# Optimization experiments

Hardware: AMD Instinct MI355X
Metric: run time of the kernel (lower is better)

Reference implementation:

```python
import jax, jax.numpy as jnp
import numpy as np

NOISE_EPS = 0.01
TOP_K = 2


def setup_inputs() -> dict:
    key = jax.random.key(0)
    k1, k2, k3, k4 = jax.random.split(key, 4)
    B, S, D, E = 4, 4096, 2048, 64
    x = jax.random.normal(k1, (B, S, D), dtype=jnp.float32)
    raw_noise = jax.random.normal(k2, (B, S, E), dtype=jnp.float32)
    # gating_mlp: single Linear(D -> E), init std=0.02, zero bias
    W_gate = 0.02 * jax.random.normal(k3, (E, D), dtype=jnp.float32)
    b_gate = jnp.zeros((E,), dtype=jnp.float32)
    # noise_projection: Linear(D -> E, bias=False), init std=1/sqrt(D)
    W_noise = (1.0 / np.sqrt(D)) * jax.random.normal(k4, (E, D), dtype=jnp.float32)
    return {"x": x, "raw_noise": raw_noise, "W_gate": W_gate, "b_gate": b_gate, "W_noise": W_noise}


def reference(x, raw_noise, W_gate, b_gate, W_noise):
    # gate logits: [B,S,E]
    logits = jnp.einsum("bsd,ed->bse", x, W_gate) + b_gate
    # noisy top-k routing (training path)
    noise_stddev = jax.nn.softplus(jnp.einsum("bsd,ed->bse", x, W_noise)) + NOISE_EPS
    noisy = logits + raw_noise * noise_stddev
    top_v, top_i = jax.lax.top_k(noisy, TOP_K)            # [B,S,K]
    top_p = jax.nn.softmax(top_v.astype(jnp.float32), axis=-1).astype(noisy.dtype)
    B, S, E = noisy.shape
    T = B * S
    flat_logits = noisy.reshape(T, E)
    flat_i = top_i.reshape(T, TOP_K)
    flat_p = top_p.reshape(T, TOP_K)
    sparse = jnp.zeros((T, E), dtype=noisy.dtype).at[jnp.arange(T)[:, None], flat_i].set(flat_p)
    # aux load-balancing loss
    indicator = (sparse > 0.0).astype(jnp.float32)
    fraction_routed = indicator.sum(axis=0) / T           # f_e
    router_probs = jax.nn.softmax(flat_logits.astype(jnp.float32), axis=-1)
    avg_prob = router_probs.mean(axis=0)                  # p_e
    aux_loss = jnp.sum(fraction_routed * avg_prob) * E
    return sparse.reshape(B, S, E), aux_loss.astype(noisy.dtype)
```

## Files before the change

### kernel.cpp

```cpp
#include <hip/hip_runtime.h>
#include <math.h>

#define TOK 16384
#define DD  2048
#define EE  64
#define MT  64
#define BKC 32
#define NKC 64
#define LDA 40

typedef _Float16 half8 __attribute__((ext_vector_type(8)));
typedef float floatx4 __attribute__((ext_vector_type(4)));

__global__ void build_wf(const float* __restrict__ Wg, const float* __restrict__ Wn,
                         _Float16* __restrict__ wf) {
  int tid  = blockIdx.x * 256 + threadIdx.x;
  int lane = tid & 63;
  int kc   = (tid >> 6) & 63;
  int ct   = tid >> 12;
  int col  = (ct & 3) * 16 + (lane & 15);
  int k    = kc * 32 + (lane >> 4) * 8;
  const float* W = (ct < 4) ? Wg : Wn;
  const float* src = W + (size_t)col * DD + k;
  float4 a = *reinterpret_cast<const float4*>(src);
  float4 b = *reinterpret_cast<const float4*>(src + 4);
  float v[8] = {a.x, a.y, a.z, a.w, b.x, b.y, b.z, b.w};
  half8 hi, lo;
#pragma unroll
  for (int j = 0; j < 8; ++j) {
    _Float16 h = (_Float16)v[j];
    hi[j] = h;
    lo[j] = (_Float16)(v[j] - (float)h);
  }
  size_t base = (((size_t)(ct * 64 + kc) * 2 + 0) * 64 + lane) * 8;
  *reinterpret_cast<half8*>(wf + base)       = hi;
  *reinterpret_cast<half8*>(wf + base + 512) = lo;
}

__global__ __launch_bounds__(256, 1)
void gating_kernel(const float* __restrict__ x, const float* __restrict__ rn,
                   const _Float16* __restrict__ wf, const float* __restrict__ bg,
                   float* __restrict__ out,
                   float* __restrict__ cnt_g, float* __restrict__ psum_g) {
  __shared__ _Float16 xs[2][2][MT * LDA];
  __shared__ float Lb[MT][129];
  __shared__ float Pb[MT][65];
  __shared__ float Rb[MT][65];
  __shared__ float Sb[MT * EE];
  __shared__ float Bgs[EE];
  __shared__ float isum[MT];
  __shared__ int   ti[MT][2];

  const int t  = threadIdx.x;
  const int w  = t >> 6;
  const int l  = t & 63;
  const int q  = l >> 4;
  const int cl = l & 15;
  const int t0 = blockIdx.x * MT;

  const int stok = t >> 2;
  const int skof = (t & 3) * 8;
  const float* xrow = x + (size_t)(t0 + stok) * DD + skof;

  floatx4 acc[4][2];
#pragma unroll
  for (int mt = 0; mt < 4; ++mt)
#pragma unroll
    for (int nt = 0; nt < 2; ++nt) acc[mt][nt] = (floatx4)0.f;

  const half8* wfp = (const half8*)wf;
  half8 Bc[2][2], Bn[2][2];

  {
    float4 a = *reinterpret_cast<const float4*>(xrow);
    float4 b = *reinterpret_cast<const float4*>(xrow + 4);
    float v[8] = {a.x, a.y, a.z, a.w, b.x, b.y, b.z, b.w};
    half8 hi, lo;
#pragma unroll
    for (int j = 0; j < 8; ++j) {
      _Float16 h = (_Float16)v[j];
      hi[j] = h;
      lo[j] = (_Float16)(v[j] - (float)h);
    }
    *reinterpret_cast<half8*>(&xs[0][0][stok * LDA + skof]) = hi;
    *reinterpret_cast<half8*>(&xs[0][1][stok * LDA + skof]) = lo;
#pragma unroll
    for (int nt = 0; nt < 2; ++nt) {
      int ct = w * 2 + nt;
#pragma unroll
      for (int s = 0; s < 2; ++s)
        Bc[nt][s] = wfp[((size_t)(ct * 64 + 0) * 2 + s) * 64 + l];
    }
  }

  for (int kc = 0; kc < NKC; ++kc) {
    const int cur = kc & 1;
    float4 pa, pb;
    const bool more = (kc < NKC - 1);
    if (more) {
      pa = *reinterpret_cast<const float4*>(xrow + (kc + 1) * BKC);
      pb = *reinterpret_cast<const float4*>(xrow + (kc + 1) * BKC + 4);
#pragma unroll
      for (int nt = 0; nt < 2; ++nt) {
        int ct = w * 2 + nt;
#pragma unroll
        for (int s = 0; s < 2; ++s)
          Bn[nt][s] = wfp[((size_t)(ct * 64 + kc + 1) * 2 + s) * 64 + l];
      }
    }
    __syncthreads();

    half8 Ah[4], Al[4];
#pragma unroll
    for (int mt = 0; mt < 4; ++mt) {
      Ah[mt] = *reinterpret_cast<const half8*>(&xs[cur][0][(mt * 16 + cl) * LDA + q * 8]);
      Al[mt] = *reinterpret_cast<const half8*>(&xs[cur][1][(mt * 16 + cl) * LDA + q * 8]);
    }
#pragma unroll
    for (int mt = 0; mt < 4; ++mt)
#pragma unroll
      for (int nt = 0; nt < 2; ++nt)
        acc[mt][nt] = __builtin_amdgcn_mfma_f32_16x16x32_f16(Ah[mt], Bc[nt][0], acc[mt][nt], 0, 0, 0);
#pragma unroll
    for (int mt = 0; mt < 4; ++mt)
#pragma unroll
      for (int nt = 0; nt < 2; ++nt)
        acc[mt][nt] = __builtin_amdgcn_mfma_f32_16x16x32_f16(Ah[mt], Bc[nt][1], acc[mt][nt], 0, 0, 0);
#pragma unroll
    for (int mt = 0; mt < 4; ++mt)
#pragma unroll
      for (int nt = 0; nt < 2; ++nt)
        acc[mt][nt] = __builtin_amdgcn_mfma_f32_16x16x32_f16(Al[mt], Bc[nt][0], acc[mt][nt], 0, 0, 0);

    if (more) {
      float v[8] = {pa.x, pa.y, pa.z, pa.w, pb.x, pb.y, pb.z, pb.w};
      half8 hi, lo;
#pragma unroll
      for (int j = 0; j < 8; ++j) {
        _Float16 h = (_Float16)v[j];
        hi[j] = h;
        lo[j] = (_Float16)(v[j] - (float)h);
      }
      *reinterpret_cast<half8*>(&xs[cur ^ 1][0][stok * LDA + skof]) = hi;
      *reinterpret_cast<half8*>(&xs[cur ^ 1][1][stok * LDA + skof]) = lo;
#pragma unroll
      for (int nt = 0; nt < 2; ++nt)
#pragma unroll
        for (int s = 0; s < 2; ++s) Bc[nt][s] = Bn[nt][s];
    }
  }

#pragma unroll
  for (int mt = 0; mt < 4; ++mt)
#pragma unroll
    for (int nt = 0; nt < 2; ++nt)
#pragma unroll
      for (int r = 0; r < 4; ++r)
        Lb[mt * 16 + q * 4 + r][w * 32 + nt * 16 + cl] = acc[mt][nt][r];

  if (t < EE) Bgs[t] = bg[t];
#pragma unroll
  for (int i = 0; i < 16; ++i) Sb[t + 256 * i] = 0.f;
#pragma unroll
  for (int i = 0; i < 16; ++i) {
    int idx = t + 256 * i;
    Rb[idx >> 6][idx & 63] = rn[(size_t)t0 * EE + idx];
  }
  __syncthreads();

  if (t < MT) {
    float v1 = -1e30f, v2 = -1e30f;
    int   i1 = 0, i2 = 0;
    float s = 0.f;
    for (int e = 0; e < EE; ++e) {
      float g  = Lb[t][e] + Bgs[e];
      float h  = Lb[t][EE + e];
      float sp = (h > 20.f) ? h : log1pf(expf(h));
      float v  = g + Rb[t][e] * (sp + 0.01f);
      float ev = expf(v);
      s += ev;
      Pb[t][e] = ev;
      if (v > v1)      { v2 = v1; i2 = i1; v1 = v; i1 = e; }
      else if (v > v2) { v2 = v;  i2 = e; }
    }
    isum[t] = 1.f / s;
    ti[t][0] = i1; ti[t][1] = i2;
    float e2 = expf(v2 - v1);
    float dn = 1.f + e2;
    Sb[t * EE + i1] = 1.f / dn;
    Sb[t * EE + i2] = e2 / dn;
  }
  __syncthreads();

#pragma unroll
  for (int i = 0; i < 16; ++i)
    out[(size_t)t0 * EE + t + 256 * i] = Sb[t + 256 * i];

  if (t < EE) {
    float s = 0.f;
    int   c = 0;
#pragma unroll
    for (int m = 0; m < MT; ++m) {
      s += Pb[m][t] * isum[m];
      c += (ti[m][0] == t) + (ti[m][1] == t);
    }
    atomicAdd(&psum_g[t], s);
    atomicAdd(&cnt_g[t], (float)c);
  }
}

__global__ void aux_kernel(const float* __restrict__ cnt_g,
                           const float* __restrict__ psum_g,
                           float* __restrict__ out) {
  int e = threadIdx.x;
  float v = cnt_g[e] * psum_g[e];
#pragma unroll
  for (int o = 32; o > 0; o >>= 1) v += __shfl_down(v, o);
  if (e == 0)
    out[(size_t)TOK * EE] = v * ((float)EE / ((float)TOK * (float)TOK));
}

extern "C" void kernel_launch(void* const* d_in, const int* in_sizes, int n_in,
                              void* d_out, int out_size, void* d_ws, size_t ws_size,
                              hipStream_t stream) {
  const float* x  = (const float*)d_in[0];
  const float* rn = (const float*)d_in[1];
  const float* Wg = (const float*)d_in[2];
  const float* bg = (const float*)d_in[3];
  const float* Wn = (const float*)d_in[4];
  float* out    = (float*)d_out;
  float* cnt_g  = (float*)d_ws;
  float* psum_g = cnt_g + EE;
  _Float16* wf  = (_Float16*)((float*)d_ws + 128);

  hipMemsetAsync(d_ws, 0, 2 * EE * sizeof(float), stream);
  build_wf<<<128, 256, 0, stream>>>(Wg, Wn, wf);
  gating_kernel<<<TOK / MT, 256, 0, stream>>>(x, rn, wf, bg, out, cnt_g, psum_g);
  aux_kernel<<<1, 64, 0, stream>>>(cnt_g, psum_g, out);
}
```

Before: 249.4 us.

## Halve token tile, fuse gating epilogue into registers, and raise occupancy

Shrinks the token tile from 64 to 32, which doubles the block count to 512, cuts shared memory through an aliased smem buffer, and sets launch bounds to two blocks per CU so more waves can hide latency. The per-element softplus, noise and exp work now runs in the MFMA accumulator registers across all threads instead of a serial 64-thread loop. The dense output is written with vectorized stores computed from top-k indices. Each block still reads the full weight panel, so weight traffic per token doubles, and the 16-wide column mapping changes the channel layout.

```diff
diff --git a/kernel.cpp b/kernel.cpp
--- a/kernel.cpp
+++ b/kernel.cpp
@@ -4,13 +4,14 @@
 #define TOK 16384
 #define DD  2048
 #define EE  64
-#define MT  64
+#define MT  32
 #define BKC 32
 #define NKC 64
 #define LDA 40
 
-typedef _Float16 half8 __attribute__((ext_vector_type(8)));
-typedef float floatx4 __attribute__((ext_vector_type(4)));
+typedef _Float16 half4v __attribute__((ext_vector_type(4)));
+typedef _Float16 half8  __attribute__((ext_vector_type(8)));
+typedef float    floatx4 __attribute__((ext_vector_type(4)));
 
 __global__ void build_wf(const float* __restrict__ Wg, const float* __restrict__ Wn,
                          _Float16* __restrict__ wf) {
@@ -37,34 +38,42 @@
   *reinterpret_cast<half8*>(wf + base + 512) = lo;
 }
 
-__global__ __launch_bounds__(256, 1)
+__global__ __launch_bounds__(256, 2)
 void gating_kernel(const float* __restrict__ x, const float* __restrict__ rn,
                    const _Float16* __restrict__ wf, const float* __restrict__ bg,
                    float* __restrict__ out,
                    float* __restrict__ cnt_g, float* __restrict__ psum_g) {
-  __shared__ _Float16 xs[2][2][MT * LDA];
-  __shared__ float Lb[MT][129];
-  __shared__ float Pb[MT][65];
-  __shared__ float Rb[MT][65];
-  __shared__ float Sb[MT * EE];
-  __shared__ float Bgs[EE];
-  __shared__ float isum[MT];
-  __shared__ int   ti[MT][2];
+  __shared__ char smem[17536];
+  _Float16* xs  = (_Float16*)smem;
+  float*    Vb  = (float*)smem;
+  float*    Eb  = (float*)(smem + 8448);
+  float*    isum= (float*)(smem + 16896);
+  int*      ti  = (int*)(smem + 17024);
+  float*    tp  = (float*)(smem + 17280);
 
   const int t  = threadIdx.x;
   const int w  = t >> 6;
   const int l  = t & 63;
   const int q  = l >> 4;
   const int cl = l & 15;
+  const int c  = w * 16 + cl;
   const int t0 = blockIdx.x * MT;
 
-  const int stok = t >> 2;
-  const int skof = (t & 3) * 8;
+  const int stok = t >> 3;
+  const int skof = (t & 7) * 4;
   const float* xrow = x + (size_t)(t0 + stok) * DD + skof;
 
-  floatx4 acc[4][2];
-#pragma unroll
-  for (int mt = 0; mt < 4; ++mt)
+  const float bgv = bg[c];
+  float rnv[2][4];
+#pragma unroll
+  for (int mt = 0; mt < 2; ++mt)
+#pragma unroll
+    for (int r = 0; r < 4; ++r)
+      rnv[mt][r] = rn[(size_t)(t0 + mt * 16 + q * 4 + r) * EE + c];
+
+  floatx4 acc[2][2];
+#pragma unroll
+  for (int mt = 0; mt < 2; ++mt)
 #pragma unroll
     for (int nt = 0; nt < 2; ++nt) acc[mt][nt] = (floatx4)0.f;
 
@@ -73,20 +82,19 @@
 
   {
     float4 a = *reinterpret_cast<const float4*>(xrow);
-    float4 b = *reinterpret_cast<const float4*>(xrow + 4);
-    float v[8] = {a.x, a.y, a.z, a.w, b.x, b.y, b.z, b.w};
-    half8 hi, lo;
-#pragma unroll
-    for (int j = 0; j < 8; ++j) {
+    float v[4] = {a.x, a.y, a.z, a.w};
+    half4v hi, lo;
+#pragma unroll
+    for (int j = 0; j < 4; ++j) {
       _Float16 h = (_Float16)v[j];
       hi[j] = h;
       lo[j] = (_Float16)(v[j] - (float)h);
     }
-    *reinterpret_cast<half8*>(&xs[0][0][stok * LDA + skof]) = hi;
-    *reinterpret_cast<half8*>(&xs[0][1][stok * LDA + skof]) = lo;
+    *reinterpret_cast<half4v*>(&xs[(0 * 2 + 0) * MT * LDA + stok * LDA + skof]) = hi;
+    *reinterpret_cast<half4v*>(&xs[(0 * 2 + 1) * MT * LDA + stok * LDA + skof]) = lo;
 #pragma unroll
     for (int nt = 0; nt < 2; ++nt) {
-      int ct = w * 2 + nt;
+      const int ct = w + nt * 4;
 #pragma unroll
       for (int s = 0; s < 2; ++s)
         Bc[nt][s] = wfp[((size_t)(ct * 64 + 0) * 2 + s) * 64 + l];
@@ -95,14 +103,13 @@
 
   for (int kc = 0; kc < NKC; ++kc) {
     const int cur = kc & 1;
-    float4 pa, pb;
     const bool more = (kc < NKC - 1);
+    float4 pa;
     if (more) {
       pa = *reinterpret_cast<const float4*>(xrow + (kc + 1) * BKC);
-      pb = *reinterpret_cast<const float4*>(xrow + (kc + 1) * BKC + 4);
 #pragma unroll
       for (int nt = 0; nt < 2; ++nt) {
-        int ct = w * 2 + nt;
+        const int ct = w + nt * 4;
 #pragma unroll
         for (int s = 0; s < 2; ++s)
           Bn[nt][s] = wfp[((size_t)(ct * 64 + kc + 1) * 2 + s) * 64 + l];
@@ -110,39 +117,41 @@
     }
     __syncthreads();
 
-    half8 Ah[4], Al[4];
-#pragma unroll
-    for (int mt = 0; mt < 4; ++mt) {
-      Ah[mt] = *reinterpret_cast<const half8*>(&xs[cur][0][(mt * 16 + cl) * LDA + q * 8]);
-      Al[mt] = *reinterpret_cast<const half8*>(&xs[cur][1][(mt * 16 + cl) * LDA + q * 8]);
-    }
-#pragma unroll
-    for (int mt = 0; mt < 4; ++mt)
+    half8 Ah[2], Al[2];
+#pragma unroll
+    for (int mt = 0; mt < 2; ++mt) {
+      Ah[mt] = *reinterpret_cast<const half8*>(
+          &xs[(cur * 2 + 0) * MT * LDA + (mt * 16 + cl) * LDA + q * 8]);
+      Al[mt] = *reinterpret_cast<const half8*>(
+          &xs[(cur * 2 + 1) * MT * LDA + (mt * 16 + cl) * LDA + q * 8]);
+    }
+#pragma unroll
+    for (int mt = 0; mt < 2; ++mt)
 #pragma unroll
       for (int nt = 0; nt < 2; ++nt)
         acc[mt][nt] = __builtin_amdgcn_mfma_f32_16x16x32_f16(Ah[mt], Bc[nt][0], acc[mt][nt], 0, 0, 0);
 #pragma unroll
-    for (int mt = 0; mt < 4; ++mt)
+    for (int mt = 0; mt < 2; ++mt)
 #pragma unroll
       for (int nt = 0; nt < 2; ++nt)
         acc[mt][nt] = __builtin_amdgcn_mfma_f32_16x16x32_f16(Ah[mt], Bc[nt][1], acc[mt][nt], 0, 0, 0);
 #pragma unroll
-    for (int mt = 0; mt < 4; ++mt)
+    for (int mt = 0; mt < 2; ++mt)
 #pragma unroll
       for (int nt = 0; nt < 2; ++nt)
         acc[mt][nt] = __builtin_amdgcn_mfma_f32_16x16x32_f16(Al[mt], Bc[nt][0], acc[mt][nt], 0, 0, 0);
 
     if (more) {
-      float v[8] = {pa.x, pa.y, pa.z, pa.w, pb.x, pb.y, pb.z, pb.w};
-      half8 hi, lo;
-#pragma unroll
-      for (int j = 0; j < 8; ++j) {
+      float v[4] = {pa.x, pa.y, pa.z, pa.w};
+      half4v hi, lo;
+#pragma unroll
+      for (int j = 0; j < 4; ++j) {
         _Float16 h = (_Float16)v[j];
         hi[j] = h;
         lo[j] = (_Float16)(v[j] - (float)h);
       }
-      *reinterpret_cast<half8*>(&xs[cur ^ 1][0][stok * LDA + skof]) = hi;
-      *reinterpret_cast<half8*>(&xs[cur ^ 1][1][stok * LDA + skof]) = lo;
+      *reinterpret_cast<half4v*>(&xs[((cur ^ 1) * 2 + 0) * MT * LDA + stok * LDA + skof]) = hi;
+      *reinterpret_cast<half4v*>(&xs[((cur ^ 1) * 2 + 1) * MT * LDA + stok * LDA + skof]) = lo;
 #pragma unroll
       for (int nt = 0; nt < 2; ++nt)
 #pragma unroll
@@ -150,22 +159,20 @@
     }
   }
 
-#pragma unroll
-  for (int mt = 0; mt < 4; ++mt)
-#pragma unroll
-    for (int nt = 0; nt < 2; ++nt)
-#pragma unroll
-      for (int r = 0; r < 4; ++r)
-        Lb[mt * 16 + q * 4 + r][w * 32 + nt * 16 + cl] = acc[mt][nt][r];
-
-  if (t < EE) Bgs[t] = bg[t];
-#pragma unroll
-  for (int i = 0; i < 16; ++i) Sb[t + 256 * i] = 0.f;
-#pragma unroll
-  for (int i = 0; i < 16; ++i) {
-    int idx = t + 256 * i;
-    Rb[idx >> 6][idx & 63] = rn[(size_t)t0 * EE + idx];
-  }
+  __syncthreads();
+
+#pragma unroll
+  for (int mt = 0; mt < 2; ++mt)
+#pragma unroll
+    for (int r = 0; r < 4; ++r) {
+      const int tk = mt * 16 + q * 4 + r;
+      float g  = acc[mt][0][r] + bgv;
+      float h  = acc[mt][1][r];
+      float sp = (h > 20.f) ? h : log1pf(expf(h));
+      float v  = g + rnv[mt][r] * (sp + 0.01f);
+      Vb[tk * 66 + c] = v;
+      Eb[tk * 66 + c] = expf(v);
+    }
   __syncthreads();
 
   if (t < MT) {
@@ -173,39 +180,46 @@
     int   i1 = 0, i2 = 0;
     float s = 0.f;
     for (int e = 0; e < EE; ++e) {
-      float g  = Lb[t][e] + Bgs[e];
-      float h  = Lb[t][EE + e];
-      float sp = (h > 20.f) ? h : log1pf(expf(h));
-      float v  = g + Rb[t][e] * (sp + 0.01f);
-      float ev = expf(v);
-      s += ev;
-      Pb[t][e] = ev;
+      float v = Vb[t * 66 + e];
+      s += Eb[t * 66 + e];
       if (v > v1)      { v2 = v1; i2 = i1; v1 = v; i1 = e; }
       else if (v > v2) { v2 = v;  i2 = e; }
     }
     isum[t] = 1.f / s;
-    ti[t][0] = i1; ti[t][1] = i2;
+    ti[t * 2 + 0] = i1; ti[t * 2 + 1] = i2;
     float e2 = expf(v2 - v1);
     float dn = 1.f + e2;
-    Sb[t * EE + i1] = 1.f / dn;
-    Sb[t * EE + i2] = e2 / dn;
+    tp[t * 2 + 0] = 1.f / dn;
+    tp[t * 2 + 1] = e2 / dn;
   }
   __syncthreads();
 
-#pragma unroll
-  for (int i = 0; i < 16; ++i)
-    out[(size_t)t0 * EE + t + 256 * i] = Sb[t + 256 * i];
+  {
+    const int m  = t >> 3;
+    const int c0 = (t & 7) * 8;
+    const int i1 = ti[m * 2 + 0], i2 = ti[m * 2 + 1];
+    const float p1 = tp[m * 2 + 0], p2 = tp[m * 2 + 1];
+    float o[8];
+#pragma unroll
+    for (int j = 0; j < 8; ++j) {
+      const int col = c0 + j;
+      o[j] = (col == i1) ? p1 : ((col == i2) ? p2 : 0.f);
+    }
+    float* dst = out + (size_t)(t0 + m) * EE + c0;
+    *reinterpret_cast<float4*>(dst)     = make_float4(o[0], o[1], o[2], o[3]);
+    *reinterpret_cast<float4*>(dst + 4) = make_float4(o[4], o[5], o[6], o[7]);
+  }
 
   if (t < EE) {
     float s = 0.f;
-    int   c = 0;
+    int   cn = 0;
 #pragma unroll
     for (int m = 0; m < MT; ++m) {
-      s += Pb[m][t] * isum[m];
-      c += (ti[m][0] == t) + (ti[m][1] == t);
+      s  += Eb[m * 66 + t] * isum[m];
+      cn += (ti[m * 2 + 0] == t) + (ti[m * 2 + 1] == t);
     }
     atomicAdd(&psum_g[t], s);
-    atomicAdd(&cnt_g[t], (float)c);
+    atomicAdd(&cnt_g[t], (float)cn);
   }
 }
 
```

After: 240.6 us. -3.5%, faster.
